# Kernel optimization log

Hardware: AMD Instinct MI355X
Metric: run time of the kernel (lower is better)

The kernel has to match this reference:

```python
import jax, jax.numpy as jnp
import numpy as np

B, S, D, H = 4, 1024, 1024, 16
HD = D // H
LN_EPS = 1e-5


def setup_inputs() -> dict:
    key = jax.random.key(0)
    ks = jax.random.split(key, 16)
    def lin(k, fan_in, fan_out):
        bound = 1.0 / np.sqrt(fan_in)
        kw, kb = jax.random.split(k)
        W = jax.random.uniform(kw, (fan_in, fan_out), jnp.float32, -bound, bound)
        b = jax.random.uniform(kb, (fan_out,), jnp.float32, -bound, bound)
        return W, b
    W_attn, b_attn = lin(ks[0], D, 3 * D)   # self-attn fused QKV
    W_Q, b_Q = lin(ks[1], D, D)             # cross-attn Q
    W_KV, b_KV = lin(ks[2], D, 2 * D)       # cross-attn KV
    W1, b1 = lin(ks[3], D, 4 * D)           # FFN up
    W2, b2 = lin(ks[4], 4 * D, D)           # FFN down
    return {
        'en': jax.random.normal(ks[5], (B, S, D), jnp.float32),
        'fr': jax.random.normal(ks[6], (B, S, D), jnp.float32),
        'W_attn': W_attn, 'b_attn': b_attn,
        'W_Q': W_Q, 'b_Q': b_Q, 'W_KV': W_KV, 'b_KV': b_KV,
        'ln_g': jnp.ones((D,), jnp.float32), 'ln_b': jnp.zeros((D,), jnp.float32),
        'W1': W1, 'b1': b1, 'W2': W2, 'b2': b2,
        'l_en': jax.random.randint(ks[7], (B,), 1, S + 1, jnp.int32),
        'l_fr': jax.random.randint(ks[8], (B,), 1, S + 1, jnp.int32),
    }


def _masked_softmax(s):
    # softmax with rows that may be entirely -inf -> all-zero row (torch softmax + nan_to_num)
    m = jnp.max(s, axis=-1, keepdims=True)
    m = jnp.where(jnp.isfinite(m), m, 0.0)
    e = jnp.exp(s - m)  # exp(-inf) = 0
    z = jnp.sum(e, axis=-1, keepdims=True)
    return jnp.where(z > 0, e / jnp.where(z > 0, z, 1.0), 0.0)


def _layer_norm(x, g, b):
    mu = jnp.mean(x, axis=-1, keepdims=True)
    var = jnp.mean((x - mu) ** 2, axis=-1, keepdims=True)
    return (x - mu) * jax.lax.rsqrt(var + LN_EPS) * g + b


def _attend(q, k, v, mask):
    # q,k,v: [B,H,S,hd]; mask: [B,1|H broadcastable,S,S] of {0,1}
    scores = jnp.einsum('bhqd,bhkd->bhqk', q, k) / (D ** 0.5)  # NOTE: scaled by sqrt(D), as in source
    scores = jnp.where(mask == 0, -jnp.inf, scores)
    p = _masked_softmax(scores)
    out = jnp.einsum('bhqk,bhkd->bhqd', p, v)
    return out.transpose(0, 2, 1, 3).reshape(q.shape[0], q.shape[2], D)


def _valid(l):
    return (jnp.arange(S)[None, :] < l[:, None]).astype(jnp.float32)  # [B,S]


def reference(en, fr, W_attn, b_attn, W_Q, b_Q, W_KV, b_KV, ln_g, ln_b, W1, b1, W2, b2, l_en, l_fr):
    # dropout layers are identity in eval/reference mode
    v_en, v_fr = _valid(l_en), _valid(l_fr)

    # --- masked causal self-attention on fr ---
    rc = fr
    qkv = (fr @ W_attn + b_attn).reshape(B, S, 3, H, HD).transpose(2, 0, 3, 1, 4)
    q, k, v = qkv[0], qkv[1], qkv[2]
    pad = (v_fr[:, :, None] * v_fr[:, None, :])[:, None]            # [B,1,S,S]
    causal = jnp.tril(jnp.ones((S, S), jnp.float32))[None, None]    # [1,1,S,S]
    x = _attend(q, k, v, pad * causal)
    fr2 = _layer_norm(x + rc, ln_g, ln_b)

    # --- encoder-decoder cross attention ---
    rc = fr2
    q = (fr2 @ W_Q + b_Q).reshape(B, S, H, HD).transpose(0, 2, 1, 3)
    kv = (en @ W_KV + b_KV).reshape(B, S, 2, H, HD).transpose(2, 0, 3, 1, 4)
    k, v = kv[0], kv[1]
    cross = (v_fr[:, :, None] * v_en[:, None, :])[:, None]          # [B,1,S,S]
    x = _attend(q, k, v, cross)
    fr3 = _layer_norm(x + rc, ln_g, ln_b)

    # --- FFN (Linear->ReLU->Linear) then extra ReLU, residual, LN ---
    rc = fr3
    h = jax.nn.relu(fr3 @ W1 + b1) @ W2 + b2
    h = jax.nn.relu(h)
    fr4 = _layer_norm(h + rc, ln_g, ln_b)
    return fr4
```

## Files before the change

kernel.cpp:

```cpp
#include <hip/hip_runtime.h>
#include <hip/hip_bf16.h>
#include <cstdint>
#include <cstddef>

#define S_LEN  1024
#define DMODEL 1024
#define NHEAD  16
#define HDIM   64
#define BATCH  4
#define MROWS  (BATCH * S_LEN)

typedef __bf16 bf16;
typedef __attribute__((ext_vector_type(8))) __bf16 bf16x8;
typedef __attribute__((ext_vector_type(4))) __bf16 bf16x4;
typedef __attribute__((ext_vector_type(4))) float f32x4;
typedef __attribute__((ext_vector_type(4))) unsigned int u32x4;

__device__ __forceinline__ void async_load16(const void* g, void* l) {
    __builtin_amdgcn_global_load_lds(
        (const __attribute__((address_space(1))) unsigned int*)g,
        (__attribute__((address_space(3))) unsigned int*)l,
        16, 0, 0);
}

__global__ __launch_bounds__(256)
void prep_all(const float* __restrict__ fr, bf16* __restrict__ fr_bf,
              const float* __restrict__ en, bf16* __restrict__ en_bf,
              const float* __restrict__ Wa, bf16* __restrict__ Ta,
              const float* __restrict__ Wq, bf16* __restrict__ Tq,
              const float* __restrict__ Wkv, bf16* __restrict__ Tkv,
              const float* __restrict__ W1, bf16* __restrict__ T1,
              const float* __restrict__ W2, bf16* __restrict__ T2) {
    __shared__ float t[32][33];
    int id = blockIdx.x;
    if (id < 8192) {
        const int n4 = MROWS * DMODEL / 4;
        int i = id * 256 + threadIdx.x;
        const float* in = fr; bf16* out = fr_bf;
        if (i >= n4) { i -= n4; in = en; out = en_bf; }
        f32x4 v = ((const f32x4*)in)[i];
        bf16x4 o;
#pragma unroll
        for (int e = 0; e < 4; ++e) o[e] = (bf16)v[e];
        ((bf16x4*)out)[i] = o;
        return;
    }
    id -= 8192;
    const float* W; bf16* Wt; int K, N, nx, base;
    if (id < 3072)       { W = Wa;  Wt = Ta;  K = 1024; N = 3072; nx = 96;  base = 0; }
    else if (id < 4096)  { W = Wq;  Wt = Tq;  K = 1024; N = 1024; nx = 32;  base = 3072; }
    else if (id < 6144)  { W = Wkv; Wt = Tkv; K = 1024; N = 2048; nx = 64;  base = 4096; }
    else if (id < 10240) { W = W1;  Wt = T1;  K = 1024; N = 4096; nx = 128; base = 6144; }
    else                 { W = W2;  Wt = T2;  K = 4096; N = 1024; nx = 32;  base = 10240; }
    int loc = id - base;
    int n0 = (loc % nx) * 32, k0 = (loc / nx) * 32;
    int tx = threadIdx.x & 31, ty = threadIdx.x >> 5;
#pragma unroll
    for (int j = 0; j < 4; ++j)
        t[ty + j * 8][tx] = W[(size_t)(k0 + ty + j * 8) * N + n0 + tx];
    __syncthreads();
#pragma unroll
    for (int j = 0; j < 4; ++j)
        Wt[(size_t)(n0 + ty + j * 8) * K + k0 + tx] = (bf16)t[tx][ty + j * 8];
}

__device__ __forceinline__ void gemm_acc(const bf16* __restrict__ A,
                                         const bf16* __restrict__ Bt,
                                         int Klen, int lda, int ldb,
                                         bf16* Alds, bf16* Blds,
                                         f32x4 acc[4][4]) {
    const int tid = threadIdx.x;
    const int wave = tid >> 6, lane = tid & 63;
    const int wr = wave >> 1, wc = wave & 1;
    const int lr = lane & 15, lg = lane >> 4, lk = lg * 8;
    const int srow = lane >> 2, scol = (lane & 3) * 8;

    const bf16* Aw = A + (size_t)(wave * 32 + srow) * lda + scol;
    const bf16* Bw = Bt + (size_t)(wave * 32 + srow) * ldb + scol;
    const int ldsw = (wave * 32) * 32;

    async_load16(Aw, Alds + ldsw);
    async_load16(Aw + (size_t)16 * lda, Alds + ldsw + 16 * 32);
    async_load16(Bw, Blds + ldsw);
    async_load16(Bw + (size_t)16 * ldb, Blds + ldsw + 16 * 32);
    __syncthreads();

    const int nt = Klen >> 5;
    for (int t = 0; t < nt; ++t) {
        const int cur = t & 1;
        if (t + 1 < nt) {
            const size_t k0 = (size_t)(t + 1) << 5;
            bf16* Ad = Alds + (cur ^ 1) * (128 * 32) + ldsw;
            bf16* Bd = Blds + (cur ^ 1) * (128 * 32) + ldsw;
            async_load16(Aw + k0, Ad);
            async_load16(Aw + (size_t)16 * lda + k0, Ad + 16 * 32);
            async_load16(Bw + k0, Bd);
            async_load16(Bw + (size_t)16 * ldb + k0, Bd + 16 * 32);
        }
        const bf16* Ab = Alds + cur * (128 * 32);
        const bf16* Bb = Blds + cur * (128 * 32);
        bf16x8 af[4], bfv[4];
#pragma unroll
        for (int i = 0; i < 4; ++i) {
            af[i]  = *(const bf16x8*)&Ab[(wr * 64 + i * 16 + lr) * 32 + lk];
            bfv[i] = *(const bf16x8*)&Bb[(wc * 64 + i * 16 + lr) * 32 + lk];
        }
#pragma unroll
        for (int mi = 0; mi < 4; ++mi)
#pragma unroll
            for (int ni = 0; ni < 4; ++ni)
                acc[mi][ni] = __builtin_amdgcn_mfma_f32_16x16x32_bf16(
                    af[mi], bfv[ni], acc[mi][ni], 0, 0, 0);
        __syncthreads();
    }
}

template<bool RELU>
__device__ __forceinline__ void epi_bf16(bf16* __restrict__ C, const float* __restrict__ bias,
                                         int N, int m0, int n0, f32x4 acc[4][4]) {
    const int tid = threadIdx.x;
    const int wave = tid >> 6, lane = tid & 63;
    const int wr = wave >> 1, wc = wave & 1;
    const int lr = lane & 15, lg = lane >> 4;
#pragma unroll
    for (int ni = 0; ni < 4; ++ni) {
        int n = n0 + wc * 64 + ni * 16 + lr;
        float bn = bias[n];
#pragma unroll
        for (int mi = 0; mi < 4; ++mi)
#pragma unroll
            for (int r = 0; r < 4; ++r) {
                int m = m0 + wr * 64 + mi * 16 + lg * 4 + r;
                float v = acc[mi][ni][r] + bn;
                if (RELU) v = v > 0.f ? v : 0.f;
                C[(size_t)m * N + n] = (bf16)v;
            }
    }
}

__device__ __forceinline__ bool tile_dead(const int* Lm, int m0) {
    if (!Lm) return false;
    int cap = (Lm[m0 >> 10] + 63) & ~63;
    return (m0 & 1023) >= cap;
}

template<bool RELU>
__global__ __launch_bounds__(256, 2)
void gemm_one(const bf16* __restrict__ A, const bf16* __restrict__ Bt,
              const float* __restrict__ bias, bf16* __restrict__ C,
              int N, int K, int gx, const int* __restrict__ Lm) {
    __shared__ alignas(16) bf16 Alds[2][128 * 32];
    __shared__ alignas(16) bf16 Blds[2][128 * 32];
    const int nwg = gridDim.x;
    const int flat = blockIdx.x;
    const int swz = (flat & 7) * (nwg >> 3) + (flat >> 3);
    const int m0 = (swz / gx) * 128, n0 = (swz % gx) * 128;
    if (tile_dead(Lm, m0)) return;
    f32x4 acc[4][4] = {};
    gemm_acc(A + (size_t)m0 * K, Bt + (size_t)n0 * K, K, K, K,
             &Alds[0][0], &Blds[0][0], acc);
    epi_bf16<RELU>(C, bias, N, m0, n0, acc);
}

struct GemmArgs {
    const bf16* A; const bf16* Bt; const float* bias; bf16* C;
    int N; int K; int gx; const int* Lm;
};
__global__ __launch_bounds__(256, 2)
void gemm_dual(GemmArgs g0, int nwg0, GemmArgs g1) {
    __shared__ alignas(16) bf16 Alds[2][128 * 32];
    __shared__ alignas(16) bf16 Blds[2][128 * 32];
    const int nwg = gridDim.x;
    const int flat = blockIdx.x;
    const int swz = (flat & 7) * (nwg >> 3) + (flat >> 3);
    const bool first = swz < nwg0;
    const GemmArgs g = first ? g0 : g1;
    const int f = first ? swz : swz - nwg0;
    const int m0 = (f / g.gx) * 128, n0 = (f % g.gx) * 128;
    if (tile_dead(g.Lm, m0)) return;
    f32x4 acc[4][4] = {};
    gemm_acc(g.A + (size_t)m0 * g.K, g.Bt + (size_t)n0 * g.K, g.K, g.K, g.K,
             &Alds[0][0], &Blds[0][0], acc);
    epi_bf16<false>(g.C, g.bias, g.N, m0, n0, acc);
}

__global__ __launch_bounds__(256, 2)
void gemm_splitk2(const bf16* __restrict__ A, const bf16* __restrict__ Bt,
                  float* __restrict__ P0, float* __restrict__ P1,
                  int N, int K, int gx, int nwg_half) {
    __shared__ alignas(16) bf16 Alds[2][128 * 32];
    __shared__ alignas(16) bf16 Blds[2][128 * 32];
    const int nwg = gridDim.x;
    const int flat = blockIdx.x;
    const int swz = (flat & 7) * (nwg >> 3) + (flat >> 3);
    const int kz = swz >= nwg_half ? 1 : 0;
    const int f = swz - kz * nwg_half;
    const int m0 = (f / gx) * 128, n0 = (f % gx) * 128;
    const int Kh = K >> 1;
    const size_t koff = (size_t)kz * Kh;
    f32x4 acc[4][4] = {};
    gemm_acc(A + (size_t)m0 * K + koff, Bt + (size_t)n0 * K + koff, Kh, K, K,
             &Alds[0][0], &Blds[0][0], acc);
    float* P = kz ? P1 : P0;
    const int tid = threadIdx.x;
    const int wave = tid >> 6, lane = tid & 63;
    const int wr = wave >> 1, wc = wave & 1;
    const int lr = lane & 15, lg = lane >> 4;
#pragma unroll
    for (int ni = 0; ni < 4; ++ni) {
        int n = n0 + wc * 64 + ni * 16 + lr;
#pragma unroll
        for (int mi = 0; mi < 4; ++mi)
#pragma unroll
            for (int r = 0; r < 4; ++r) {
                int m = m0 + wr * 64 + mi * 16 + lg * 4 + r;
                P[(size_t)m * N + n] = acc[mi][ni][r];
            }
    }
}

template<bool CAUSAL>
__global__ __launch_bounds__(256, 4)
void attn_flash(const bf16* __restrict__ Qp, int qs,
                const bf16* __restrict__ Kp, int ks,
                const bf16* __restrict__ Vp, int vs,
                const int* __restrict__ Lq, const int* __restrict__ Lk,
                bf16* __restrict__ Op) {
    __shared__ alignas(16) bf16 Klds[64 * 64];
    __shared__ alignas(16) bf16 Vt[64 * 64];
    __shared__ alignas(16) bf16 Plds[4][16 * 64];

    const int tid = threadIdx.x;
    const int wave = tid >> 6, lane = tid & 63;
    const int qt = blockIdx.x, h = blockIdx.y, b = blockIdx.z;
    const int q0 = qt * 64;
    const int lq = Lq[b], lk = Lk[b];
    const int lr = lane & 15, lg = lane >> 4;

    if (q0 >= lq) {
#pragma unroll
        for (int dt = 0; dt < 4; ++dt)
#pragma unroll
            for (int r = 0; r < 4; ++r) {
                int q = q0 + wave * 16 + lg * 4 + r;
                Op[(size_t)(b * S_LEN + q) * DMODEL + h * HDIM + dt * 16 + lr] = (bf16)0.f;
            }
        return;
    }

    char* KldsB = (char*)Klds;
    char* VtB = (char*)Vt;
    char* PldsB = (char*)&Plds[wave][0];

    bf16x8 aq[2];
    {
        const bf16* qrow = Qp + (size_t)(b * S_LEN + q0 + wave * 16 + lr) * qs + h * HDIM;
        aq[0] = *(const bf16x8*)(qrow + 0 + lg * 8);
        aq[1] = *(const bf16x8*)(qrow + 32 + lg * 8);
    }

    f32x4 o[4] = {};
    float m_run[4], l_run[4];
#pragma unroll
    for (int r = 0; r < 4; ++r) { m_run[r] = -INFINITY; l_run[r] = 0.f; }

    int kv_end = CAUSAL ? (q0 + 64) : S_LEN;
    int lk_cap = (lk + 63) & ~63;
    if (kv_end > lk_cap) kv_end = lk_cap;

    const int vk = lane;
    const int vd0 = wave * 16;

    for (int kk0 = 0; kk0 < kv_end; kk0 += 64) {
#pragma unroll
        for (int c = 0; c < 2; ++c) {
            int rloc = c * 8 + (lane >> 3);
            int row = wave * 16 + rloc;
            int chunk = (lane & 7) ^ (rloc & 7);
            async_load16(Kp + (size_t)(b * S_LEN + kk0 + row) * ks + h * HDIM + chunk * 8,
                         KldsB + (size_t)(wave * 16 + c * 8) * 128);
        }
        {
            const bf16* vsrc = Vp + (size_t)(b * S_LEN + kk0 + vk) * vs + h * HDIM + vd0;
            bf16x8 v0 = *(const bf16x8*)vsrc;
            bf16x8 v1 = *(const bf16x8*)(vsrc + 8);
#pragma unroll
            for (int e = 0; e < 8; ++e) {
                int d0 = vd0 + e, d1 = vd0 + 8 + e;
                *(bf16*)(VtB + (((size_t)d0 * 128 + vk * 2) ^ ((d0 & 7) << 4))) = v0[e];
                *(bf16*)(VtB + (((size_t)d1 * 128 + vk * 2) ^ ((d1 & 7) << 4))) = v1[e];
            }
        }
        __syncthreads();

        f32x4 sa[4];
#pragma unroll
        for (int kt = 0; kt < 4; ++kt) {
            int row = kt * 16 + lr;
            f32x4 z = {};
#pragma unroll
            for (int ds_ = 0; ds_ < 2; ++ds_) {
                bf16x8 bk = *(const bf16x8*)(KldsB +
                    (((size_t)row * 128 + ds_ * 64 + lg * 16) ^ ((row & 7) << 4)));
                z = __builtin_amdgcn_mfma_f32_16x16x32_bf16(aq[ds_], bk, z, 0, 0, 0);
            }
            sa[kt] = z;
        }

        float p[4][4];
#pragma unroll
        for (int r = 0; r < 4; ++r) {
            int q = q0 + wave * 16 + lg * 4 + r;
            float best = -INFINITY;
#pragma unroll
            for (int kt = 0; kt < 4; ++kt) {
                int kk = kk0 + kt * 16 + lr;
                float s = sa[kt][r] * 0.03125f;
                bool ok = (q < lq) && (kk < lk) && (!CAUSAL || kk <= q);
                s = ok ? s : -INFINITY;
                p[kt][r] = s;
                best = fmaxf(best, s);
            }
#pragma unroll
            for (int msk = 1; msk < 16; msk <<= 1)
                best = fmaxf(best, __shfl_xor(best, msk));
            float mn = fmaxf(m_run[r], best);
            float alpha = (m_run[r] == -INFINITY) ? 0.0f : __expf(m_run[r] - mn);
            float rs = 0.f;
#pragma unroll
            for (int kt = 0; kt < 4; ++kt) {
                float s = p[kt][r];
                float e = (s == -INFINITY) ? 0.f : __expf(s - mn);
                p[kt][r] = e;
                rs += e;
            }
#pragma unroll
            for (int msk = 1; msk < 16; msk <<= 1)
                rs += __shfl_xor(rs, msk);
            l_run[r] = l_run[r] * alpha + rs;
            m_run[r] = mn;
#pragma unroll
            for (int dt = 0; dt < 4; ++dt) o[dt][r] *= alpha;
        }

#pragma unroll
        for (int kt = 0; kt < 4; ++kt)
#pragma unroll
            for (int r = 0; r < 4; ++r) {
                int ql = lg * 4 + r, kkl = kt * 16 + lr;
                *(bf16*)(PldsB + (((size_t)ql * 128 + kkl * 2) ^ ((ql & 7) << 4))) =
                    (bf16)p[kt][r];
            }
        bf16x8 pa[2];
#pragma unroll
        for (int ksl = 0; ksl < 2; ++ksl)
            pa[ksl] = *(const bf16x8*)(PldsB +
                (((size_t)lr * 128 + ksl * 64 + lg * 16) ^ ((lr & 7) << 4)));

#pragma unroll
        for (int dt = 0; dt < 4; ++dt) {
            int row = dt * 16 + lr;
#pragma unroll
            for (int ksl = 0; ksl < 2; ++ksl) {
                bf16x8 bv = *(const bf16x8*)(VtB +
                    (((size_t)row * 128 + ksl * 64 + lg * 16) ^ ((row & 7) << 4)));
                o[dt] = __builtin_amdgcn_mfma_f32_16x16x32_bf16(pa[ksl], bv, o[dt], 0, 0, 0);
            }
        }
        __syncthreads();
    }

#pragma unroll
    for (int dt = 0; dt < 4; ++dt) {
#pragma unroll
        for (int r = 0; r < 4; ++r) {
            int q = q0 + wave * 16 + lg * 4 + r;
            float denom = l_run[r];
            float val = denom > 0.f ? o[dt][r] / denom : 0.f;
            Op[(size_t)(b * S_LEN + q) * DMODEL + h * HDIM + dt * 16 + lr] = (bf16)val;
        }
    }
}

__global__ __launch_bounds__(256)
void ln_kernel(const bf16* __restrict__ x, const float* __restrict__ rc,
               const float* __restrict__ g, const float* __restrict__ beta,
               float* __restrict__ yf, bf16* __restrict__ yb) {
    const int row = blockIdx.x;
    const int tid = threadIdx.x;
    const int wave = tid >> 6, lane = tid & 63;
    const bf16* xr = x + (size_t)row * DMODEL;
    const float* rr = rc + (size_t)row * DMODEL;

    float v[4];
    {
        bf16x4 xv = *(const bf16x4*)(xr + tid * 4);
        f32x4 rv = *(const f32x4*)(rr + tid * 4);
#pragma unroll
        for (int i = 0; i < 4; ++i) v[i] = (float)xv[i] + rv[i];
    }
    float s = v[0] + v[1] + v[2] + v[3];
    float s2 = v[0] * v[0] + v[1] * v[1] + v[2] * v[2] + v[3] * v[3];
#pragma unroll
    for (int msk = 1; msk < 64; msk <<= 1) {
        s += __shfl_xor(s, msk);
        s2 += __shfl_xor(s2, msk);
    }
    __shared__ float red[8];
    if (lane == 0) { red[wave] = s; red[4 + wave] = s2; }
    __syncthreads();
    float ts = red[0] + red[1] + red[2] + red[3];
    float ts2 = red[4] + red[5] + red[6] + red[7];
    float mean = ts * (1.f / DMODEL);
    float var = ts2 * (1.f / DMODEL) - mean * mean;
    float inv = rsqrtf(var + 1e-5f);
#pragma unroll
    for (int i = 0; i < 4; ++i) {
        int c = tid * 4 + i;
        float yv = (v[i] - mean) * inv * g[c] + beta[c];
        if (yf) yf[(size_t)row * DMODEL + c] = yv;
        if (yb) yb[(size_t)row * DMODEL + c] = (bf16)yv;
    }
}

__global__ __launch_bounds__(256)
void ln_splitk(const float* __restrict__ P0, const float* __restrict__ P1,
               const float* __restrict__ bias, const float* __restrict__ rc,
               const float* __restrict__ g, const float* __restrict__ beta,
               float* __restrict__ yf) {
    const int row = blockIdx.x;
    const int tid = threadIdx.x;
    const int wave = tid >> 6, lane = tid & 63;
    const size_t off = (size_t)row * DMODEL + tid * 4;

    f32x4 a = *(const f32x4*)(P0 + off);
    f32x4 bb = *(const f32x4*)(P1 + off);
    f32x4 bi = *(const f32x4*)(bias + tid * 4);
    f32x4 rv = *(const f32x4*)(rc + off);
    float v[4];
#pragma unroll
    for (int i = 0; i < 4; ++i) {
        float h = a[i] + bb[i] + bi[i];
        h = h > 0.f ? h : 0.f;
        v[i] = h + rv[i];
    }
    float s = v[0] + v[1] + v[2] + v[3];
    float s2 = v[0] * v[0] + v[1] * v[1] + v[2] * v[2] + v[3] * v[3];
#pragma unroll
    for (int msk = 1; msk < 64; msk <<= 1) {
        s += __shfl_xor(s, msk);
        s2 += __shfl_xor(s2, msk);
    }
    __shared__ float red[8];
    if (lane == 0) { red[wave] = s; red[4 + wave] = s2; }
    __syncthreads();
    float ts = red[0] + red[1] + red[2] + red[3];
    float ts2 = red[4] + red[5] + red[6] + red[7];
    float mean = ts * (1.f / DMODEL);
    float var = ts2 * (1.f / DMODEL) - mean * mean;
    float inv = rsqrtf(var + 1e-5f);
#pragma unroll
    for (int i = 0; i < 4; ++i) {
        int c = tid * 4 + i;
        yf[(size_t)row * DMODEL + c] = (v[i] - mean) * inv * g[c] + beta[c];
    }
}

extern "C" void kernel_launch(void* const* d_in, const int* in_sizes, int n_in,
                              void* d_out, int out_size, void* d_ws, size_t ws_size,
                              hipStream_t stream) {
    const float* en     = (const float*)d_in[0];
    const float* fr     = (const float*)d_in[1];
    const float* W_attn = (const float*)d_in[2];
    const float* b_attn = (const float*)d_in[3];
    const float* W_Q    = (const float*)d_in[4];
    const float* b_Q    = (const float*)d_in[5];
    const float* W_KV   = (const float*)d_in[6];
    const float* b_KV   = (const float*)d_in[7];
    const float* ln_g   = (const float*)d_in[8];
    const float* ln_b   = (const float*)d_in[9];
    const float* W1     = (const float*)d_in[10];
    const float* b1     = (const float*)d_in[11];
    const float* W2     = (const float*)d_in[12];
    const float* b2     = (const float*)d_in[13];
    const int* l_en     = (const int*)d_in[14];
    const int* l_fr     = (const int*)d_in[15];
    float* out = (float*)d_out;

    char* ws = (char*)d_ws;
    const size_t MB = (size_t)1 << 20;
    bf16* Wt_attn = (bf16*)(ws + 0);
    bf16* Wt_Q    = (bf16*)(ws + 6 * MB);
    bf16* Wt_KV   = (bf16*)(ws + 8 * MB);
    bf16* Wt_1    = (bf16*)(ws + 12 * MB);
    bf16* Wt_2    = (bf16*)(ws + 20 * MB);
    bf16* fr_bf   = (bf16*)(ws + 28 * MB);
    bf16* en_bf   = (bf16*)(ws + 36 * MB);
    bf16* bigA    = (bf16*)(ws + 44 * MB);
    bf16* xbuf    = (bf16*)(ws + 76 * MB);
    float* fr2    = (float*)(ws + 84 * MB);
    float* fr3    = (float*)(ws + 100 * MB);
    bf16* fbx     = (bf16*)(ws + 116 * MB);
    float* P0 = (float*)(ws + 0);
    float* P1 = (float*)(ws + 28 * MB);
    bf16* kvc = (bf16*)(ws + 100 * MB);

    dim3 blk(256);

    prep_all<<<dim3(22528), blk, 0, stream>>>(fr, fr_bf, en, en_bf,
        W_attn, Wt_attn, W_Q, Wt_Q, W_KV, Wt_KV, W1, Wt_1, W2, Wt_2);

    bf16* qkv = bigA;
    GemmArgs gq{fr_bf, Wt_attn, b_attn, qkv, 3072, 1024, 24, l_fr};
    GemmArgs gk{en_bf, Wt_KV, b_KV, kvc, 2048, 1024, 16, l_en};
    gemm_dual<<<dim3(1280), blk, 0, stream>>>(gq, 768, gk);

    attn_flash<true><<<dim3(16, NHEAD, BATCH), blk, 0, stream>>>(
        qkv, 3072, qkv + 1024, 3072, qkv + 2048, 3072, l_fr, l_fr, xbuf);
    ln_kernel<<<dim3(4096), blk, 0, stream>>>(xbuf, fr, ln_g, ln_b, fr2, fbx);

    bf16* qc = bigA;
    gemm_one<false><<<dim3(256), blk, 0, stream>>>(fbx, Wt_Q, b_Q, qc, 1024, 1024, 8, l_fr);
    attn_flash<false><<<dim3(16, NHEAD, BATCH), blk, 0, stream>>>(
        qc, 1024, kvc, 2048, kvc + 1024, 2048, l_fr, l_en, xbuf);
    ln_kernel<<<dim3(4096), blk, 0, stream>>>(xbuf, fr2, ln_g, ln_b, fr3, fbx);

    bf16* h = bigA;
    gemm_one<true><<<dim3(1024), blk, 0, stream>>>(fbx, Wt_1, b1, h, 4096, 1024, 32, nullptr);
    gemm_splitk2<<<dim3(512), blk, 0, stream>>>(h, Wt_2, P0, P1, 1024, 4096, 8, 256);
    ln_splitk<<<dim3(4096), blk, 0, stream>>>(P0, P1, b2, fr3, ln_g, ln_b, out);
}
```

Baseline: 306.4 us.

## Add 256x256-tile 8-wave GEMM for QKV/KV and FFN-up projections

```diff
diff --git a/kernel.cpp b/kernel.cpp
--- a/kernel.cpp
+++ b/kernel.cpp
@@ -64,6 +64,180 @@
         Wt[(size_t)(n0 + ty + j * 8) * K + k0 + tx] = (bf16)t[tx][ty + j * 8];
 }
 
+__device__ __forceinline__ void st_A(char* smem, const bf16* A, int K, int m0,
+                                     int buf, int sm, int tile, int t) {
+    char* dst = smem + (size_t)(buf * 2 + sm) * 16384 + (size_t)(t & ~63) * 16;
+#pragma unroll
+    for (int j = 0; j < 2; ++j) {
+        int ra = j * 64 + (t >> 3);
+        int gr = m0 + ((ra >> 6) << 7) + sm * 64 + (ra & 63);
+        int c = (t & 7) ^ ((t >> 3) & 7);
+        async_load16(A + (size_t)gr * K + tile * 64 + c * 8, dst + j * 8192);
+    }
+}
+__device__ __forceinline__ void st_B(char* smem, const bf16* B, int K, int n0,
+                                     int buf, int sn, int tile, int t) {
+    char* dst = smem + 65536 + (size_t)(buf * 2 + sn) * 16384 + (size_t)(t & ~63) * 16;
+#pragma unroll
+    for (int j = 0; j < 2; ++j) {
+        int rb = j * 64 + (t >> 3);
+        int gr = n0 + ((rb >> 5) << 6) + sn * 32 + (rb & 31);
+        int c = (t & 7) ^ ((t >> 3) & 7);
+        async_load16(B + (size_t)gr * K + tile * 64 + c * 8, dst + j * 8192);
+    }
+}
+__device__ __forceinline__ void rd_A(const char* Ar, int wm, int lr, int lg,
+                                     bf16x8 (&a)[4][2]) {
+#pragma unroll
+    for (int mi = 0; mi < 4; ++mi)
+#pragma unroll
+        for (int ks = 0; ks < 2; ++ks)
+            a[mi][ks] = *(const bf16x8*)(Ar + (wm * 64 + mi * 16 + lr) * 128 +
+                                         ((ks * 64 + lg * 16) ^ ((lr & 7) << 4)));
+}
+__device__ __forceinline__ void rd_B(const char* Br, int wn, int lr, int lg,
+                                     bf16x8 (&b)[2][2]) {
+#pragma unroll
+    for (int ni = 0; ni < 2; ++ni)
+#pragma unroll
+        for (int ks = 0; ks < 2; ++ks)
+            b[ni][ks] = *(const bf16x8*)(Br + (wn * 32 + ni * 16 + lr) * 128 +
+                                         ((ks * 64 + lg * 16) ^ ((lr & 7) << 4)));
+}
+template<int SM, int SN>
+__device__ __forceinline__ void mm16(const bf16x8 (&a)[4][2], const bf16x8 (&b)[2][2],
+                                     f32x4 (&acc)[8][4]) {
+#pragma unroll
+    for (int mi = 0; mi < 4; ++mi)
+#pragma unroll
+        for (int ni = 0; ni < 2; ++ni)
+#pragma unroll
+            for (int ks = 0; ks < 2; ++ks)
+                acc[SM * 4 + mi][SN * 2 + ni] = __builtin_amdgcn_mfma_f32_16x16x32_bf16(
+                    a[mi][ks], b[ni][ks], acc[SM * 4 + mi][SN * 2 + ni], 0, 0, 0);
+}
+
+struct GemmArgs {
+    const bf16* A; const bf16* Bt; const float* bias; bf16* C;
+    int N; int K; int gx; const int* Lm; int relu;
+};
+
+#define BARRIER()  __builtin_amdgcn_s_barrier()
+#define LGKM0()    asm volatile("s_waitcnt lgkmcnt(0)" ::: "memory")
+#define PRIO(x)    __builtin_amdgcn_s_setprio(x)
+
+__global__ __launch_bounds__(512, 2)
+void gemm256_dual(GemmArgs g0, int nwg0, GemmArgs g1) {
+    __shared__ alignas(16) char smem[131072];
+    const int tid = threadIdx.x;
+    const int wave = tid >> 6, lane = tid & 63;
+    const int wm = wave >> 2, wn = wave & 3;
+    const int lr = lane & 15, lg = lane >> 4;
+
+    const int nwg = gridDim.x;
+    const int flat = blockIdx.x;
+    const int swz = (flat & 7) * (nwg >> 3) + (flat >> 3);
+    const bool first = swz < nwg0;
+    const GemmArgs g = first ? g0 : g1;
+    const int f = first ? swz : swz - nwg0;
+    const int m0 = (f / g.gx) * 256, n0 = (f % g.gx) * 256;
+    if (g.Lm) {
+        int cap = (g.Lm[m0 >> 10] + 63) & ~63;
+        if ((m0 & 1023) >= cap) return;
+    }
+    const int K = g.K;
+    const int nkt = K >> 6;
+
+    const char* Ap[2][2] = {
+        { smem, smem + 16384 }, { smem + 32768, smem + 49152 } };
+    const char* Bp[2][2] = {
+        { smem + 65536, smem + 81920 }, { smem + 98304, smem + 114688 } };
+
+    bf16x8 a[4][2];
+    bf16x8 b[2][2];
+    f32x4 acc[8][4] = {};
+
+    st_A(smem, g.A, K, m0, 0, 0, 0, tid);
+    st_B(smem, g.Bt, K, n0, 0, 0, 0, tid);
+    st_A(smem, g.A, K, m0, 0, 1, 0, tid);
+    st_B(smem, g.Bt, K, n0, 0, 1, 0, tid);
+    st_A(smem, g.A, K, m0, 1, 0, 1, tid);
+    st_B(smem, g.Bt, K, n0, 1, 0, 1, tid);
+    asm volatile("s_waitcnt vmcnt(4)" ::: "memory");
+    BARRIER();
+
+    for (int T = 0; T < nkt; T += 2) {
+        const bool sE = (T + 2) < nkt, sO = (T + 3) < nkt;
+        rd_A(Ap[0][0], wm, lr, lg, a);
+        rd_B(Bp[0][0], wn, lr, lg, b);
+        st_A(smem, g.A, K, m0, 1, 1, T + 1, tid);
+        BARRIER(); LGKM0();
+        PRIO(1); mm16<0, 0>(a, b, acc); PRIO(0);
+        BARRIER();
+        rd_B(Bp[0][1], wn, lr, lg, b);
+        st_B(smem, g.Bt, K, n0, 1, 1, T + 1, tid);
+        BARRIER(); LGKM0();
+        PRIO(1); mm16<0, 1>(a, b, acc); PRIO(0);
+        BARRIER();
+        rd_A(Ap[0][1], wm, lr, lg, a);
+        rd_B(Bp[0][0], wn, lr, lg, b);
+        if (sE) st_A(smem, g.A, K, m0, 0, 0, T + 2, tid);
+        BARRIER(); LGKM0();
+        PRIO(1); mm16<1, 0>(a, b, acc); PRIO(0);
+        BARRIER();
+        rd_B(Bp[0][1], wn, lr, lg, b);
+        if (sE) {
+            st_B(smem, g.Bt, K, n0, 0, 0, T + 2, tid);
+            asm volatile("s_waitcnt vmcnt(4)" ::: "memory");
+        } else {
+            asm volatile("s_waitcnt vmcnt(0)" ::: "memory");
+        }
+        BARRIER(); LGKM0();
+        PRIO(1); mm16<1, 1>(a, b, acc); PRIO(0);
+        BARRIER();
+        rd_A(Ap[1][0], wm, lr, lg, a);
+        rd_B(Bp[1][0], wn, lr, lg, b);
+        if (sE) st_A(smem, g.A, K, m0, 0, 1, T + 2, tid);
+        BARRIER(); LGKM0();
+        PRIO(1); mm16<0, 0>(a, b, acc); PRIO(0);
+        BARRIER();
+        rd_B(Bp[1][1], wn, lr, lg, b);
+        if (sE) st_B(smem, g.Bt, K, n0, 0, 1, T + 2, tid);
+        BARRIER(); LGKM0();
+        PRIO(1); mm16<0, 1>(a, b, acc); PRIO(0);
+        BARRIER();
+        rd_A(Ap[1][1], wm, lr, lg, a);
+        rd_B(Bp[1][0], wn, lr, lg, b);
+        if (sO) st_A(smem, g.A, K, m0, 1, 0, T + 3, tid);
+        BARRIER(); LGKM0();
+        PRIO(1); mm16<1, 0>(a, b, acc); PRIO(0);
+        BARRIER();
+        rd_B(Bp[1][1], wn, lr, lg, b);
+        if (sO) {
+            st_B(smem, g.Bt, K, n0, 1, 0, T + 3, tid);
+            asm volatile("s_waitcnt vmcnt(4)" ::: "memory");
+        }
+        BARRIER(); LGKM0();
+        PRIO(1); mm16<1, 1>(a, b, acc); PRIO(0);
+        BARRIER();
+    }
+
+#pragma unroll
+    for (int ni = 0; ni < 4; ++ni) {
+        int n = n0 + wn * 64 + ni * 16 + lr;
+        float bn = g.bias[n];
+#pragma unroll
+        for (int mi = 0; mi < 8; ++mi)
+#pragma unroll
+            for (int r = 0; r < 4; ++r) {
+                int m = m0 + wm * 128 + mi * 16 + lg * 4 + r;
+                float v = acc[mi][ni][r] + bn;
+                if (g.relu) v = v > 0.f ? v : 0.f;
+                g.C[(size_t)m * g.N + n] = (bf16)v;
+            }
+    }
+}
+
 __device__ __forceinline__ void gemm_acc(const bf16* __restrict__ A,
                                          const bf16* __restrict__ Bt,
                                          int Klen, int lda, int ldb,
@@ -160,28 +334,6 @@
     gemm_acc(A + (size_t)m0 * K, Bt + (size_t)n0 * K, K, K, K,
              &Alds[0][0], &Blds[0][0], acc);
     epi_bf16<RELU>(C, bias, N, m0, n0, acc);
-}
-
-struct GemmArgs {
-    const bf16* A; const bf16* Bt; const float* bias; bf16* C;
-    int N; int K; int gx; const int* Lm;
-};
-__global__ __launch_bounds__(256, 2)
-void gemm_dual(GemmArgs g0, int nwg0, GemmArgs g1) {
-    __shared__ alignas(16) bf16 Alds[2][128 * 32];
-    __shared__ alignas(16) bf16 Blds[2][128 * 32];
-    const int nwg = gridDim.x;
-    const int flat = blockIdx.x;
-    const int swz = (flat & 7) * (nwg >> 3) + (flat >> 3);
-    const bool first = swz < nwg0;
-    const GemmArgs g = first ? g0 : g1;
-    const int f = first ? swz : swz - nwg0;
-    const int m0 = (f / g.gx) * 128, n0 = (f % g.gx) * 128;
-    if (tile_dead(g.Lm, m0)) return;
-    f32x4 acc[4][4] = {};
-    gemm_acc(g.A + (size_t)m0 * g.K, g.Bt + (size_t)n0 * g.K, g.K, g.K, g.K,
-             &Alds[0][0], &Blds[0][0], acc);
-    epi_bf16<false>(g.C, g.bias, g.N, m0, n0, acc);
 }
 
 __global__ __launch_bounds__(256, 2)
@@ -511,9 +663,9 @@
         W_attn, Wt_attn, W_Q, Wt_Q, W_KV, Wt_KV, W1, Wt_1, W2, Wt_2);
 
     bf16* qkv = bigA;
-    GemmArgs gq{fr_bf, Wt_attn, b_attn, qkv, 3072, 1024, 24, l_fr};
-    GemmArgs gk{en_bf, Wt_KV, b_KV, kvc, 2048, 1024, 16, l_en};
-    gemm_dual<<<dim3(1280), blk, 0, stream>>>(gq, 768, gk);
+    GemmArgs gq{fr_bf, Wt_attn, b_attn, qkv, 3072, 1024, 12, l_fr, 0};
+    GemmArgs gk{en_bf, Wt_KV, b_KV, kvc, 2048, 1024, 8, l_en, 0};
+    gemm256_dual<<<dim3(320), dim3(512), 0, stream>>>(gq, 192, gk);
 
     attn_flash<true><<<dim3(16, NHEAD, BATCH), blk, 0, stream>>>(
         qkv, 3072, qkv + 1024, 3072, qkv + 2048, 3072, l_fr, l_fr, xbuf);
@@ -526,7 +678,8 @@
     ln_kernel<<<dim3(4096), blk, 0, stream>>>(xbuf, fr2, ln_g, ln_b, fr3, fbx);
 
     bf16* h = bigA;
-    gemm_one<true><<<dim3(1024), blk, 0, stream>>>(fbx, Wt_1, b1, h, 4096, 1024, 32, nullptr);
+    GemmArgs gf{fbx, Wt_1, b1, h, 4096, 1024, 16, nullptr, 1};
+    gemm256_dual<<<dim3(256), dim3(512), 0, stream>>>(gf, 256, gf);
     gemm_splitk2<<<dim3(512), blk, 0, stream>>>(h, Wt_2, P0, P1, 1024, 4096, 8, 256);
     ln_splitk<<<dim3(4096), blk, 0, stream>>>(P0, P1, b2, fr3, ln_g, ln_b, out);
 }
```

After: 312.4 us. No clear change (+2.0%).

## Widen flash-attention KV tile to 128 and alias P buffer onto K LDS

Applied to the files above, without the earlier changes.

```diff
diff --git a/kernel.cpp b/kernel.cpp
--- a/kernel.cpp
+++ b/kernel.cpp
@@ -226,9 +226,8 @@
                 const bf16* __restrict__ Vp, int vs,
                 const int* __restrict__ Lq, const int* __restrict__ Lk,
                 bf16* __restrict__ Op) {
-    __shared__ alignas(16) bf16 Klds[64 * 64];
-    __shared__ alignas(16) bf16 Vt[64 * 64];
-    __shared__ alignas(16) bf16 Plds[4][16 * 64];
+    __shared__ alignas(16) bf16 Klds[128 * 64];
+    __shared__ alignas(16) bf16 Vt[64 * 128];
 
     const int tid = threadIdx.x;
     const int wave = tid >> 6, lane = tid & 63;
@@ -250,7 +249,7 @@
 
     char* KldsB = (char*)Klds;
     char* VtB = (char*)Vt;
-    char* PldsB = (char*)&Plds[wave][0];
+    char* PB = KldsB + wave * 4096;
 
     bf16x8 aq[2];
     {
@@ -265,60 +264,57 @@
     for (int r = 0; r < 4; ++r) { m_run[r] = -INFINITY; l_run[r] = 0.f; }
 
     int kv_end = CAUSAL ? (q0 + 64) : S_LEN;
-    int lk_cap = (lk + 63) & ~63;
-    if (kv_end > lk_cap) kv_end = lk_cap;
-
-    const int vk = lane;
-    const int vd0 = wave * 16;
-
-    for (int kk0 = 0; kk0 < kv_end; kk0 += 64) {
-#pragma unroll
-        for (int c = 0; c < 2; ++c) {
-            int rloc = c * 8 + (lane >> 3);
-            int row = wave * 16 + rloc;
-            int chunk = (lane & 7) ^ (rloc & 7);
+    if (kv_end > lk) kv_end = lk;
+    kv_end = (kv_end + 127) & ~127;
+
+    for (int kk0 = 0; kk0 < kv_end; kk0 += 128) {
+#pragma unroll
+        for (int c = 0; c < 4; ++c) {
+            int row = wave * 32 + c * 8 + (lane >> 3);
+            int chunk = (lane & 7) ^ ((lane >> 3) & 7);
             async_load16(Kp + (size_t)(b * S_LEN + kk0 + row) * ks + h * HDIM + chunk * 8,
-                         KldsB + (size_t)(wave * 16 + c * 8) * 128);
-        }
-        {
-            const bf16* vsrc = Vp + (size_t)(b * S_LEN + kk0 + vk) * vs + h * HDIM + vd0;
+                         KldsB + (size_t)(wave * 32 + c * 8) * 128);
+        }
+#pragma unroll
+        for (int half = 0; half < 2; ++half) {
+            int vkk = half * 64 + lane;
+            const bf16* vsrc = Vp + (size_t)(b * S_LEN + kk0 + vkk) * vs + h * HDIM + wave * 16;
             bf16x8 v0 = *(const bf16x8*)vsrc;
             bf16x8 v1 = *(const bf16x8*)(vsrc + 8);
 #pragma unroll
             for (int e = 0; e < 8; ++e) {
-                int d0 = vd0 + e, d1 = vd0 + 8 + e;
-                *(bf16*)(VtB + (((size_t)d0 * 128 + vk * 2) ^ ((d0 & 7) << 4))) = v0[e];
-                *(bf16*)(VtB + (((size_t)d1 * 128 + vk * 2) ^ ((d1 & 7) << 4))) = v1[e];
+                int d0 = wave * 16 + e, d1 = wave * 16 + 8 + e;
+                *(bf16*)(VtB + (((size_t)d0 * 256 + vkk * 2) ^ ((d0 & 7) << 4))) = v0[e];
+                *(bf16*)(VtB + (((size_t)d1 * 256 + vkk * 2) ^ ((d1 & 7) << 4))) = v1[e];
             }
         }
         __syncthreads();
 
-        f32x4 sa[4];
-#pragma unroll
-        for (int kt = 0; kt < 4; ++kt) {
+        f32x4 sa[8];
+#pragma unroll
+        for (int kt = 0; kt < 8; ++kt) {
             int row = kt * 16 + lr;
             f32x4 z = {};
-#pragma unroll
-            for (int ds_ = 0; ds_ < 2; ++ds_) {
-                bf16x8 bk = *(const bf16x8*)(KldsB +
-                    (((size_t)row * 128 + ds_ * 64 + lg * 16) ^ ((row & 7) << 4)));
-                z = __builtin_amdgcn_mfma_f32_16x16x32_bf16(aq[ds_], bk, z, 0, 0, 0);
-            }
+            bf16x8 bk0 = *(const bf16x8*)(KldsB +
+                (((size_t)row * 128 + 0 + lg * 16) ^ ((row & 7) << 4)));
+            bf16x8 bk1 = *(const bf16x8*)(KldsB +
+                (((size_t)row * 128 + 64 + lg * 16) ^ ((row & 7) << 4)));
+            z = __builtin_amdgcn_mfma_f32_16x16x32_bf16(aq[0], bk0, z, 0, 0, 0);
+            z = __builtin_amdgcn_mfma_f32_16x16x32_bf16(aq[1], bk1, z, 0, 0, 0);
             sa[kt] = z;
         }
 
-        float p[4][4];
 #pragma unroll
         for (int r = 0; r < 4; ++r) {
             int q = q0 + wave * 16 + lg * 4 + r;
             float best = -INFINITY;
 #pragma unroll
-            for (int kt = 0; kt < 4; ++kt) {
+            for (int kt = 0; kt < 8; ++kt) {
                 int kk = kk0 + kt * 16 + lr;
                 float s = sa[kt][r] * 0.03125f;
                 bool ok = (q < lq) && (kk < lk) && (!CAUSAL || kk <= q);
                 s = ok ? s : -INFINITY;
-                p[kt][r] = s;
+                sa[kt][r] = s;
                 best = fmaxf(best, s);
             }
 #pragma unroll
@@ -328,10 +324,10 @@
             float alpha = (m_run[r] == -INFINITY) ? 0.0f : __expf(m_run[r] - mn);
             float rs = 0.f;
 #pragma unroll
-            for (int kt = 0; kt < 4; ++kt) {
-                float s = p[kt][r];
+            for (int kt = 0; kt < 8; ++kt) {
+                float s = sa[kt][r];
                 float e = (s == -INFINITY) ? 0.f : __expf(s - mn);
-                p[kt][r] = e;
+                sa[kt][r] = e;
                 rs += e;
             }
 #pragma unroll
@@ -342,28 +338,29 @@
 #pragma unroll
             for (int dt = 0; dt < 4; ++dt) o[dt][r] *= alpha;
         }
-
-#pragma unroll
-        for (int kt = 0; kt < 4; ++kt)
+        __syncthreads();
+
+#pragma unroll
+        for (int kt = 0; kt < 8; ++kt)
 #pragma unroll
             for (int r = 0; r < 4; ++r) {
                 int ql = lg * 4 + r, kkl = kt * 16 + lr;
-                *(bf16*)(PldsB + (((size_t)ql * 128 + kkl * 2) ^ ((ql & 7) << 4))) =
-                    (bf16)p[kt][r];
-            }
-        bf16x8 pa[2];
-#pragma unroll
-        for (int ksl = 0; ksl < 2; ++ksl)
-            pa[ksl] = *(const bf16x8*)(PldsB +
-                (((size_t)lr * 128 + ksl * 64 + lg * 16) ^ ((lr & 7) << 4)));
+                *(bf16*)(PB + (((size_t)ql * 256 + kkl * 2) ^ ((ql & 7) << 4))) =
+                    (bf16)sa[kt][r];
+            }
+        bf16x8 pa[4];
+#pragma unroll
+        for (int ksl = 0; ksl < 4; ++ksl)
+            pa[ksl] = *(const bf16x8*)(PB +
+                (((size_t)lr * 256 + ksl * 64 + lg * 16) ^ ((lr & 7) << 4)));
 
 #pragma unroll
         for (int dt = 0; dt < 4; ++dt) {
             int row = dt * 16 + lr;
 #pragma unroll
-            for (int ksl = 0; ksl < 2; ++ksl) {
+            for (int ksl = 0; ksl < 4; ++ksl) {
                 bf16x8 bv = *(const bf16x8*)(VtB +
-                    (((size_t)row * 128 + ksl * 64 + lg * 16) ^ ((row & 7) << 4)));
+                    (((size_t)row * 256 + ksl * 64 + lg * 16) ^ ((row & 7) << 4)));
                 o[dt] = __builtin_amdgcn_mfma_f32_16x16x32_bf16(pa[ksl], bv, o[dt], 0, 0, 0);
             }
         }
```

Result: slower. 415.4 us (+35.6%).
